# Kernel optimization log

Measured on AMD Instinct MI355X. Metric: run time of the kernel, lower is better.

## Reference

```python
import jax, jax.numpy as jnp
import numpy as np

N_CAM, N_PTS, N_OBS = 2000, 500000, 5000000


def setup_inputs() -> dict:
    key = jax.random.key(0)
    k1, k2, k3, k4, k5, k6 = jax.random.split(key, 6)
    # SE3 poses: [tx, ty, tz, qx, qy, qz, qw] (pypose layout), unit quaternions
    t = jax.random.normal(k1, (N_CAM, 3), dtype=jnp.float32) * 5.0
    t = t.at[:, 2].set(jax.random.uniform(k2, (N_CAM,), minval=100.0, maxval=200.0))
    q = jax.random.normal(k3, (N_CAM, 4), dtype=jnp.float32)
    q = q / jnp.linalg.norm(q, axis=-1, keepdims=True)
    poses = jnp.concatenate([t, q], axis=-1)  # [N_CAM, 7]
    points = jax.random.normal(k4, (N_PTS, 3), dtype=jnp.float32) * 5.0  # [N_PTS, 3]
    # Pinhole intrinsics
    K = jnp.array([[1000.0, 0.0, 640.0], [0.0, 1000.0, 360.0], [0.0, 0.0, 1.0]], dtype=jnp.float32)
    observes = jax.random.normal(k5, (N_OBS, 2), dtype=jnp.float32) * 100.0 + 500.0
    ki, kj = jax.random.split(k6)
    cidx = jax.random.randint(ki, (N_OBS,), 0, N_CAM, dtype=jnp.int64)
    pidx = jax.random.randint(kj, (N_OBS,), 0, N_PTS, dtype=jnp.int64)
    return {"observes": observes, "K": K, "poses": poses, "points": points, "cidx": cidx, "pidx": pidx}


def _se3_act(pose7, pts):
    # pose7: [N,7] (t, q) with q=(x,y,z,w); pts: [N,3]
    t = pose7[:, :3]
    qv = pose7[:, 3:6]
    qw = pose7[:, 6:7]
    # p' = p + 2 * qv x (qv x p + w p) + t   (unit-quaternion rotation)
    uv = jnp.cross(qv, pts)
    return pts + 2.0 * jnp.cross(qv, uv + qw * pts) + t


def reference(observes, K, poses, points, cidx, pidx):
    p_cam = _se3_act(poses[cidx], points[pidx])  # [N_OBS, 3] camera-frame points
    img = p_cam @ K.T                            # [N_OBS, 3] homogeneous pixels
    projs = img[:, :2] / img[:, 2:3]             # [N_OBS, 2]
    return (projs - observes).reshape(-1)        # [N_OBS * 2]
```

## Files before the change

### kernel.cpp

```cpp
#include <hip/hip_runtime.h>


typedef float    vfloat4 __attribute__((ext_vector_type(4)));
typedef int      vint4   __attribute__((ext_vector_type(4)));
typedef _Float16 vhalf4  __attribute__((ext_vector_type(4)));
typedef _Float16 vhalf8  __attribute__((ext_vector_type(8)));

#define MAX_CAM 2000

__global__ __launch_bounds__(256) void pack_points_h(
    const float* __restrict__ src, vhalf4* __restrict__ dst, int n_pts)
{
    int i = blockIdx.x * blockDim.x + threadIdx.x;
    if (i >= n_pts) return;
    const float* s = src + 3 * i;
    vhalf4 v = {(_Float16)s[0], (_Float16)s[1], (_Float16)s[2], (_Float16)0.0f};
    dst[i] = v;
}

__global__ __launch_bounds__(256) void pack_poses_h(
    const float* __restrict__ src, vhalf8* __restrict__ dst, int n_cam)
{
    int i = blockIdx.x * blockDim.x + threadIdx.x;
    if (i >= n_cam) return;
    const float* s = src + 7 * i;
    vhalf8 v = {(_Float16)s[0], (_Float16)s[1], (_Float16)s[2],
                (_Float16)s[3], (_Float16)s[4], (_Float16)s[5],
                (_Float16)s[6], (_Float16)0.0f};
    dst[i] = v;
}

__global__ __launch_bounds__(512) void resid_h4(
    const float*  __restrict__ obs,
    const float*  __restrict__ Kmat,
    const vhalf8* __restrict__ poses_h,
    const vhalf4* __restrict__ points_h,
    const int*    __restrict__ cidx,
    const int*    __restrict__ pidx,
    float*        __restrict__ out,
    int n, int n_cam)
{
    __shared__ vhalf8 sposes[MAX_CAM];

    for (int r = threadIdx.x; r < n_cam; r += blockDim.x)
        sposes[r] = poses_h[r];
    __syncthreads();

    int t = blockIdx.x * blockDim.x + threadIdx.x;
    int base = t * 4;

    float fx = Kmat[0], cx = Kmat[2];
    float fy = Kmat[4], cy = Kmat[5];

    if (base + 4 <= n) {
        vint4   c4  = __builtin_nontemporal_load((const vint4*)(cidx + base));
        vint4   p4  = __builtin_nontemporal_load((const vint4*)(pidx + base));
        vfloat4 o01 = __builtin_nontemporal_load((const vfloat4*)(obs + 2 * base));
        vfloat4 o23 = __builtin_nontemporal_load((const vfloat4*)(obs + 2 * base + 4));

        int cc[4] = {c4.x, c4.y, c4.z, c4.w};
        int pp[4] = {p4.x, p4.y, p4.z, p4.w};

        vhalf4 P[4];
        #pragma unroll
        for (int k = 0; k < 4; ++k) P[k] = points_h[pp[k]];

        vhalf8 Q[4];
        #pragma unroll
        for (int k = 0; k < 4; ++k) Q[k] = sposes[cc[k]];

        float res[8];
        #pragma unroll
        for (int k = 0; k < 4; ++k) {
            float px = (float)P[k].x, py = (float)P[k].y, pz = (float)P[k].z;
            float tx = (float)Q[k][0], ty = (float)Q[k][1], tz = (float)Q[k][2];
            float qx = (float)Q[k][3], qy = (float)Q[k][4],
                  qz = (float)Q[k][5], qw = (float)Q[k][6];

            float ux = qy * pz - qz * py;
            float uy = qz * px - qx * pz;
            float uz = qx * py - qy * px;
            float wx = ux + qw * px;
            float wy = uy + qw * py;
            float wz = uz + qw * pz;
            float ccx = qy * wz - qz * wy;
            float ccy = qz * wx - qx * wz;
            float ccz = qx * wy - qy * wx;
            float X = px + 2.0f * ccx + tx;
            float Y = py + 2.0f * ccy + ty;
            float Z = pz + 2.0f * ccz + tz;

            float invz = 1.0f / Z;
            res[2 * k]     = fx * X * invz + cx;
            res[2 * k + 1] = fy * Y * invz + cy;
        }

        vfloat4 r0 = {res[0] - o01.x, res[1] - o01.y, res[2] - o01.z, res[3] - o01.w};
        vfloat4 r1 = {res[4] - o23.x, res[5] - o23.y, res[6] - o23.z, res[7] - o23.w};
        __builtin_nontemporal_store(r0, (vfloat4*)(out + 2 * base));
        __builtin_nontemporal_store(r1, (vfloat4*)(out + 2 * base + 4));
    } else {
        for (int i = base; i < n; ++i) {
            vhalf4 P = points_h[pidx[i]];
            vhalf8 Q = sposes[cidx[i]];
            float px = (float)P.x, py = (float)P.y, pz = (float)P.z;
            float tx = (float)Q[0], ty = (float)Q[1], tz = (float)Q[2];
            float qx = (float)Q[3], qy = (float)Q[4], qz = (float)Q[5], qw = (float)Q[6];

            float ux = qy * pz - qz * py;
            float uy = qz * px - qx * pz;
            float uz = qx * py - qy * px;
            float wx = ux + qw * px;
            float wy = uy + qw * py;
            float wz = uz + qw * pz;
            float ccx = qy * wz - qz * wy;
            float ccy = qz * wx - qx * wz;
            float ccz = qx * wy - qy * wx;
            float X = px + 2.0f * ccx + tx;
            float Y = py + 2.0f * ccy + ty;
            float Z = pz + 2.0f * ccz + tz;

            float invz = 1.0f / Z;
            out[2 * i]     = fx * X * invz + cx - obs[2 * i];
            out[2 * i + 1] = fy * Y * invz + cy - obs[2 * i + 1];
        }
    }
}

__global__ __launch_bounds__(256) void resid_fallback(
    const float* __restrict__ obs, const float* __restrict__ Kmat,
    const float* __restrict__ poses, const float* __restrict__ points,
    const int* __restrict__ cidx, const int* __restrict__ pidx,
    float* __restrict__ out, int n)
{
    int i = blockIdx.x * blockDim.x + threadIdx.x;
    if (i >= n) return;
    const float* ps = poses + 7 * cidx[i];
    const float* pt = points + 3 * pidx[i];
    float px = pt[0], py = pt[1], pz = pt[2];
    float tx = ps[0], ty = ps[1], tz = ps[2];
    float qx = ps[3], qy = ps[4], qz = ps[5], qw = ps[6];
    float ux = qy * pz - qz * py;
    float uy = qz * px - qx * pz;
    float uz = qx * py - qy * px;
    float wx = ux + qw * px;
    float wy = uy + qw * py;
    float wz = uz + qw * pz;
    float ccx = qy * wz - qz * wy;
    float ccy = qz * wx - qx * wz;
    float ccz = qx * wy - qy * wx;
    float X = px + 2.0f * ccx + tx;
    float Y = py + 2.0f * ccy + ty;
    float Z = pz + 2.0f * ccz + tz;
    float invz = 1.0f / Z;
    out[2 * i]     = Kmat[0] * X * invz + Kmat[2] - obs[2 * i];
    out[2 * i + 1] = Kmat[4] * Y * invz + Kmat[5] - obs[2 * i + 1];
}

extern "C" void kernel_launch(void* const* d_in, const int* in_sizes, int n_in,
                              void* d_out, int out_size, void* d_ws, size_t ws_size,
                              hipStream_t stream) {
    const float* obs    = (const float*)d_in[0];
    const float* Kmat   = (const float*)d_in[1];
    const float* poses  = (const float*)d_in[2];
    const float* points = (const float*)d_in[3];
    const int*   cidx   = (const int*)d_in[4];
    const int*   pidx   = (const int*)d_in[5];
    float*       out    = (float*)d_out;

    int n     = in_sizes[4];
    int n_cam = in_sizes[2] / 7;
    int n_pts = in_sizes[3] / 3;

    size_t pts_bytes  = (size_t)n_pts * sizeof(vhalf4);
    size_t pose_bytes = (size_t)n_cam * sizeof(vhalf8);

    if (ws_size < pts_bytes + pose_bytes || n_cam > MAX_CAM) {
        resid_fallback<<<(n + 255) / 256, 256, 0, stream>>>(
            obs, Kmat, poses, points, cidx, pidx, out, n);
        return;
    }

    vhalf4* points_h = (vhalf4*)d_ws;
    vhalf8* poses_h  = (vhalf8*)((char*)d_ws + pts_bytes);

    pack_points_h<<<(n_pts + 255) / 256, 256, 0, stream>>>(points, points_h, n_pts);
    pack_poses_h<<<(n_cam + 255) / 256, 256, 0, stream>>>(poses, poses_h, n_cam);

    int block = 512;
    int per_block = block * 4;
    int grid = (n + per_block - 1) / per_block;
    resid_h4<<<grid, block, 0, stream>>>(
        obs, Kmat, poses_h, points_h, cidx, pidx, out, n, n_cam);
}
```

Measured before the change: 163.5 us.

## Use persistent grid-stride loop with software-prefetched index loads

Replaces the one-chunk-per-thread launch with a fixed 1024-block persistent grid that walks the observations in a grid-stride loop. Each iteration prefetches the next chunk's camera and point indices so the dependent gather for the current chunk overlaps the next index load. Because each block now does many chunks, the 2000-entry pose table is loaded into shared memory far fewer times overall. The cost is fewer resident waves for hiding latency, and the tail of fewer than four elements is handled serially by a single thread.

```diff
diff --git a/kernel.cpp b/kernel.cpp
--- a/kernel.cpp
+++ b/kernel.cpp
@@ -30,7 +30,7 @@
     dst[i] = v;
 }
 
-__global__ __launch_bounds__(512) void resid_h4(
+__global__ __launch_bounds__(512) void resid_pipe(
     const float*  __restrict__ obs,
     const float*  __restrict__ Kmat,
     const vhalf8* __restrict__ poses_h,
@@ -46,29 +46,44 @@
         sposes[r] = poses_h[r];
     __syncthreads();
 
-    int t = blockIdx.x * blockDim.x + threadIdx.x;
-    int base = t * 4;
-
     float fx = Kmat[0], cx = Kmat[2];
     float fy = Kmat[4], cy = Kmat[5];
 
-    if (base + 4 <= n) {
-        vint4   c4  = __builtin_nontemporal_load((const vint4*)(cidx + base));
-        vint4   p4  = __builtin_nontemporal_load((const vint4*)(pidx + base));
+    int nchunk = n >> 2;
+    int tot    = gridDim.x * blockDim.x;
+    int i      = blockIdx.x * blockDim.x + threadIdx.x;
+
+    vint4 c_cur = {0, 0, 0, 0}, p_cur = {0, 0, 0, 0};
+    if (i < nchunk) {
+        c_cur = __builtin_nontemporal_load((const vint4*)(cidx + 4 * i));
+        p_cur = __builtin_nontemporal_load((const vint4*)(pidx + 4 * i));
+    }
+
+    while (i < nchunk) {
+        int base  = 4 * i;
+        int inext = i + tot;
+
+        vhalf4 P0 = points_h[p_cur.x];
+        vhalf4 P1 = points_h[p_cur.y];
+        vhalf4 P2 = points_h[p_cur.z];
+        vhalf4 P3 = points_h[p_cur.w];
+
         vfloat4 o01 = __builtin_nontemporal_load((const vfloat4*)(obs + 2 * base));
         vfloat4 o23 = __builtin_nontemporal_load((const vfloat4*)(obs + 2 * base + 4));
 
-        int cc[4] = {c4.x, c4.y, c4.z, c4.w};
-        int pp[4] = {p4.x, p4.y, p4.z, p4.w};
-
-        vhalf4 P[4];
-        #pragma unroll
-        for (int k = 0; k < 4; ++k) P[k] = points_h[pp[k]];
-
-        vhalf8 Q[4];
-        #pragma unroll
-        for (int k = 0; k < 4; ++k) Q[k] = sposes[cc[k]];
-
+        vint4 c_nxt = c_cur, p_nxt = p_cur;
+        if (inext < nchunk) {
+            c_nxt = __builtin_nontemporal_load((const vint4*)(cidx + 4 * inext));
+            p_nxt = __builtin_nontemporal_load((const vint4*)(pidx + 4 * inext));
+        }
+
+        vhalf8 Q0 = sposes[c_cur.x];
+        vhalf8 Q1 = sposes[c_cur.y];
+        vhalf8 Q2 = sposes[c_cur.z];
+        vhalf8 Q3 = sposes[c_cur.w];
+
+        vhalf4 P[4]  = {P0, P1, P2, P3};
+        vhalf8 Q[4]  = {Q0, Q1, Q2, Q3};
         float res[8];
         #pragma unroll
         for (int k = 0; k < 4; ++k) {
@@ -99,10 +114,16 @@
         vfloat4 r1 = {res[4] - o23.x, res[5] - o23.y, res[6] - o23.z, res[7] - o23.w};
         __builtin_nontemporal_store(r0, (vfloat4*)(out + 2 * base));
         __builtin_nontemporal_store(r1, (vfloat4*)(out + 2 * base + 4));
-    } else {
-        for (int i = base; i < n; ++i) {
-            vhalf4 P = points_h[pidx[i]];
-            vhalf8 Q = sposes[cidx[i]];
+
+        i = inext;
+        c_cur = c_nxt;
+        p_cur = p_nxt;
+    }
+
+    if (blockIdx.x == 0 && threadIdx.x == 0) {
+        for (int j = nchunk * 4; j < n; ++j) {
+            vhalf4 P = points_h[pidx[j]];
+            vhalf8 Q = sposes[cidx[j]];
             float px = (float)P.x, py = (float)P.y, pz = (float)P.z;
             float tx = (float)Q[0], ty = (float)Q[1], tz = (float)Q[2];
             float qx = (float)Q[3], qy = (float)Q[4], qz = (float)Q[5], qw = (float)Q[6];
@@ -121,8 +142,8 @@
             float Z = pz + 2.0f * ccz + tz;
 
             float invz = 1.0f / Z;
-            out[2 * i]     = fx * X * invz + cx - obs[2 * i];
-            out[2 * i + 1] = fy * Y * invz + cy - obs[2 * i + 1];
+            out[2 * j]     = fx * X * invz + cx - obs[2 * j];
+            out[2 * j + 1] = fy * Y * invz + cy - obs[2 * j + 1];
         }
     }
 }
@@ -188,8 +209,7 @@
     pack_poses_h<<<(n_cam + 255) / 256, 256, 0, stream>>>(poses, poses_h, n_cam);
 
     int block = 512;
-    int per_block = block * 4;
-    int grid = (n + per_block - 1) / per_block;
-    resid_h4<<<grid, block, 0, stream>>>(
+    int grid  = 1024;
+    resid_pipe<<<grid, block, 0, stream>>>(
         obs, Kmat, poses_h, points_h, cidx, pidx, out, n, n_cam);
 }
```

New measurement: 163.3 us. Within noise of the previous version (-0.1%).
